# Kernel tuning notes

Measured on AMD Instinct MI355X. Metric: run time of the kernel, lower is better.

Reference implementation:

```python
import jax, jax.numpy as jnp
import numpy as np

N = 50000      # nodes
E = 800000     # edges
F = 64         # in_channels == out_channels
ED = 16        # edge_dim
G = 64         # graphs in batch
L = 2          # numLayers
BN_EPS = 1e-5
STD_EPS = 1e-5
AGG_DIM = F * 4 * 3  # 4 aggregators x 3 scalers


def setup_inputs() -> dict:
    key = jax.random.key(0)
    ks = jax.random.split(key, 12)
    r = lambda k, shp, fan: (jax.random.normal(k, shp, jnp.float32) / np.sqrt(fan)).astype(jnp.float32)
    return dict(
        x=jax.random.normal(ks[0], (N, F), jnp.float32),
        edge_attr=jax.random.normal(ks[1], (E, ED), jnp.float32),
        We=r(ks[2], (L, ED, F), ED), be=jnp.zeros((L, F), jnp.float32),
        Wpre=r(ks[3], (L, 3 * F, F), 3 * F), bpre=jnp.zeros((L, F), jnp.float32),
        Wpost=r(ks[4], (L, F + AGG_DIM, F), F + AGG_DIM), bpost=jnp.zeros((L, F), jnp.float32),
        Wlin=r(ks[5], (L, F, F), F), blin=jnp.zeros((L, F), jnp.float32),
        gamma=jnp.ones((L, F), jnp.float32), beta=jnp.zeros((L, F), jnp.float32),
        W1=r(ks[6], (F, 40), F), b1=jnp.zeros((40,), jnp.float32),
        W2=r(ks[7], (40, 1), 40), b2=jnp.zeros((1,), jnp.float32),
        edge_index=jax.random.randint(ks[8], (2, E), 0, N),
        batch=jnp.sort(jax.random.randint(ks[9], (N,), 0, G)),
    )


def _ceal_conv(x, src, dst, edge_attr, We, be, Wpre, bpre, Wpost, bpost, Wlin, blin, deg, amp, att):
    # PNA-style conv, towers=1, pre_layers=post_layers=1
    e = edge_attr @ We + be                                              # [E,F]
    h = jnp.concatenate([x[dst], x[src], e], axis=-1) @ Wpre + bpre      # [E,F]
    degc = jnp.maximum(deg, 1.0)[:, None]
    mean = jax.ops.segment_sum(h, dst, num_segments=N) / degc
    sq = jax.ops.segment_sum(h * h, dst, num_segments=N) / degc
    std = jnp.sqrt(jax.nn.relu(sq - mean * mean) + STD_EPS)
    has = (deg > 0)[:, None]
    mn = jnp.where(has, jax.ops.segment_min(h, dst, num_segments=N), 0.0)
    mx = jnp.where(has, jax.ops.segment_max(h, dst, num_segments=N), 0.0)
    aggs = jnp.concatenate([mean, mn, mx, std], axis=-1)                 # [N,4F]
    scaled = jnp.concatenate([aggs, aggs * amp[:, None], aggs * att[:, None]], axis=-1)  # [N,12F]
    out = jnp.concatenate([x, scaled], axis=-1) @ Wpost + bpost          # [N,F]
    return out @ Wlin + blin


def _bn(x, gamma, beta):
    mu = x.mean(0)
    var = x.var(0)  # biased, as torch BatchNorm training-mode normalization
    return (x - mu) * jax.lax.rsqrt(var + BN_EPS) * gamma + beta


def reference(x, edge_attr, We, be, Wpre, bpre, Wpost, bpost, Wlin, blin,
              gamma, beta, W1, b1, W2, b2, edge_index, batch):
    src, dst = edge_index[0], edge_index[1]
    deg = jax.ops.segment_sum(jnp.ones((E,), jnp.float32), dst, num_segments=N)
    avg_log = jnp.mean(jnp.log(deg + 1.0))
    logd = jnp.log(jnp.maximum(deg, 1.0) + 1.0)
    amp = logd / avg_log
    att = avg_log / logd
    for l in range(L):
        x = _ceal_conv(x, src, dst, edge_attr, We[l], be[l], Wpre[l], bpre[l],
                       Wpost[l], bpost[l], Wlin[l], blin[l], deg, amp, att)
        x = jax.nn.relu(_bn(x, gamma[l], beta[l]))
    cnt = jnp.maximum(jax.ops.segment_sum(jnp.ones((N,), jnp.float32), batch, num_segments=G), 1.0)
    gm = jax.ops.segment_sum(x, batch, num_segments=G) / cnt[:, None]    # global_mean_pool [G,F]
    return jax.nn.relu(gm @ W1 + b1) @ W2 + b2                           # [G,1]
```

## Files before the change

kernel.cpp:

```cpp
#include <hip/hip_runtime.h>
#include <math.h>
#include <float.h>

#define NN 50000
#define EE 800000
#define FF 64
#define EDIM 16
#define GG 64
#define NB64 782
#define NSB 196

typedef short bf16x8 __attribute__((ext_vector_type(8)));
typedef float f32x4 __attribute__((ext_vector_type(4)));

__device__ inline unsigned short bf_rne(float v) {
  unsigned int u = __float_as_uint(v);
  unsigned int r = (u + 0x7FFFu + ((u >> 16) & 1u)) >> 16;
  return (unsigned short)r;
}
__device__ inline float bf_up(unsigned short h) {
  return __uint_as_float(((unsigned int)h) << 16);
}
__device__ inline void split4(float4 v, ushort4& h, ushort4& l) {
  h.x = bf_rne(v.x); h.y = bf_rne(v.y); h.z = bf_rne(v.z); h.w = bf_rne(v.w);
  l.x = bf_rne(v.x - bf_up(h.x));
  l.y = bf_rne(v.y - bf_up(h.y));
  l.z = bf_rne(v.z - bf_up(h.z));
  l.w = bf_rne(v.w - bf_up(h.w));
}
__device__ inline float blo(unsigned int u) { return __uint_as_float(u << 16); }
__device__ inline float bhi(unsigned int u) { return __uint_as_float(u & 0xFFFF0000u); }

__global__ void k_deg(const int* __restrict__ eidx, int* __restrict__ deg) {
  int e = blockIdx.x * 256 + threadIdx.x;
  if (e < EE) atomicAdd(&deg[eidx[EE + e]], 1);
}

__global__ __launch_bounds__(256) void k_scanA(const int* __restrict__ deg, int* __restrict__ offsets,
                                               int* __restrict__ bsum, float* __restrict__ lsum) {
  __shared__ int ws[4];
  __shared__ float lw[4];
  int t = threadIdx.x;
  int lane = t & 63;
  int wv = t >> 6;
  int i = blockIdx.x * 256 + t;
  int v = (i < NN) ? deg[i] : 0;
  float lg = (i < NN) ? logf((float)v + 1.0f) : 0.0f;
  int x = v;
  #pragma unroll
  for (int o = 1; o < 64; o <<= 1) {
    int y = __shfl_up(x, o);
    if (lane >= o) x += y;
  }
  #pragma unroll
  for (int o = 1; o < 64; o <<= 1) lg += __shfl_xor(lg, o);
  if (lane == 63) ws[wv] = x;
  if (lane == 0) lw[wv] = lg;
  __syncthreads();
  int pre = 0;
  for (int k = 0; k < wv; k++) pre += ws[k];
  if (i < NN) offsets[i] = pre + x - v;
  if (t == 0) {
    bsum[blockIdx.x] = ws[0] + ws[1] + ws[2] + ws[3];
    lsum[blockIdx.x] = lw[0] + lw[1] + lw[2] + lw[3];
  }
}

__global__ __launch_bounds__(256) void k_scanB(const int* __restrict__ bsum, const float* __restrict__ lsum,
                                               int* __restrict__ bpref, float* __restrict__ meta,
                                               float* __restrict__ scbA) {
  __shared__ int ws[4];
  __shared__ float lw[4];
  int t = threadIdx.x;
  int lane = t & 63;
  int wv = t >> 6;
  int v = (t < NSB) ? bsum[t] : 0;
  float lg = (t < NSB) ? lsum[t] : 0.0f;
  int x = v;
  #pragma unroll
  for (int o = 1; o < 64; o <<= 1) {
    int y = __shfl_up(x, o);
    if (lane >= o) x += y;
  }
  #pragma unroll
  for (int o = 1; o < 64; o <<= 1) lg += __shfl_xor(lg, o);
  if (lane == 63) ws[wv] = x;
  if (lane == 0) lw[wv] = lg;
  __syncthreads();
  int pre = 0;
  for (int k = 0; k < wv; k++) pre += ws[k];
  if (t < NSB) bpref[t] = pre + x - v;
  if (t == 0) meta[0] = (lw[0] + lw[1] + lw[2] + lw[3]) / (float)NN;
  if (t < 64) { scbA[t] = 1.0f; scbA[64 + t] = 0.0f; }
  if (t == 0) scbA[128] = -FLT_MAX;
}

__global__ __launch_bounds__(256) void k_scanC(int* __restrict__ offsets, const int* __restrict__ bpref,
                                               const int* __restrict__ deg, const float* __restrict__ meta,
                                               float* __restrict__ amp, float* __restrict__ att) {
  int i = blockIdx.x * 256 + threadIdx.x;
  if (i < NN) {
    offsets[i] += bpref[blockIdx.x];
    float d = (float)deg[i];
    float avg = meta[0];
    float logd = logf(fmaxf(d, 1.0f) + 1.0f);
    amp[i] = logd / avg;
    att[i] = avg / logd;
  }
  if (i == 0) offsets[NN] = EE;
}

__global__ void k_scatter(const int* __restrict__ eidx, const int* __restrict__ offsets,
                          int* __restrict__ cursor, int* __restrict__ srcs,
                          const float* __restrict__ eattr, unsigned int* __restrict__ PermEA) {
  int e = blockIdx.x * 256 + threadIdx.x;
  if (e < EE) {
    int s = eidx[e];
    int d = eidx[EE + e];
    int pos = offsets[d] + atomicAdd(&cursor[d], 1);
    srcs[pos] = s;
    const float4* ep = (const float4*)(eattr + (size_t)e * EDIM);
    float4 q0 = ep[0], q1 = ep[1], q2 = ep[2], q3 = ep[3];
    uint4 pa, pb;
    pa.x = (unsigned)bf_rne(q0.x) | ((unsigned)bf_rne(q0.y) << 16);
    pa.y = (unsigned)bf_rne(q0.z) | ((unsigned)bf_rne(q0.w) << 16);
    pa.z = (unsigned)bf_rne(q1.x) | ((unsigned)bf_rne(q1.y) << 16);
    pa.w = (unsigned)bf_rne(q1.z) | ((unsigned)bf_rne(q1.w) << 16);
    pb.x = (unsigned)bf_rne(q2.x) | ((unsigned)bf_rne(q2.y) << 16);
    pb.y = (unsigned)bf_rne(q2.z) | ((unsigned)bf_rne(q2.w) << 16);
    pb.z = (unsigned)bf_rne(q3.x) | ((unsigned)bf_rne(q3.y) << 16);
    pb.w = (unsigned)bf_rne(q3.z) | ((unsigned)bf_rne(q3.w) << 16);
    ((uint4*)PermEA)[(size_t)pos * 2] = pa;
    ((uint4*)PermEA)[(size_t)pos * 2 + 1] = pb;
  }
}

__global__ __launch_bounds__(256) void k_prep2(const float* __restrict__ We, const float* __restrict__ be,
                                               const float* __restrict__ Wpre, const float* __restrict__ bpre,
                                               const float* __restrict__ Wpost, const float* __restrict__ bpost,
                                               const float* __restrict__ Wlin, const float* __restrict__ blin,
                                               unsigned short* __restrict__ MwT_h, unsigned short* __restrict__ MwT_l,
                                               float* __restrict__ bconst,
                                               unsigned short* __restrict__ WcT_h, unsigned short* __restrict__ WcT_l,
                                               unsigned short* __restrict__ WxT_h, unsigned short* __restrict__ WxT_l,
                                               float* __restrict__ bcomb) {
  int id = blockIdx.x * 256 + threadIdx.x;
  if (id < 53248) {
    int k = id >> 6, f = id & 63;
    float a = 0.0f;
    for (int j = 0; j < FF; j++) a += Wpost[(size_t)k * FF + j] * Wlin[j * FF + f];
    unsigned short h = bf_rne(a);
    WcT_h[f * 832 + k] = h;
    WcT_l[f * 832 + k] = bf_rne(a - bf_up(h));
  } else if (id < 61440) {
    int lid = id - 53248;
    int j = lid >> 6, k = lid & 63;
    float v = (j < 64) ? Wpre[k * FF + j] : Wpre[(64 + k) * FF + (j - 64)];
    unsigned short h = bf_rne(v);
    WxT_h[j * 64 + k] = h;
    WxT_l[j * 64 + k] = bf_rne(v - bf_up(h));
  } else if (id < 62464) {
    int lid = id - 61440;
    int k = lid >> 6, f = lid & 63;
    float a = 0.0f;
    for (int j = 0; j < FF; j++) a += We[k * FF + j] * Wpre[(128 + j) * FF + f];
    unsigned short h = bf_rne(a);
    int ct = f & 3, jcol = f >> 2;
    MwT_h[(ct * 16 + jcol) * 16 + k] = h;
    MwT_l[(ct * 16 + jcol) * 16 + k] = bf_rne(a - bf_up(h));
  } else {
    int f = threadIdx.x;
    if (blockIdx.x == 244 && f < 64) {
      float b = bpre[f];
      for (int j = 0; j < FF; j++) b += be[j] * Wpre[(128 + j) * FF + f];
      bconst[f] = b;
      float c = blin[f];
      for (int j = 0; j < FF; j++) c += bpost[j] * Wlin[j * FF + f];
      bcomb[f] = c;
    }
  }
}

__global__ __launch_bounds__(256) void k_xform(const float* __restrict__ x, const float* __restrict__ scb,
                                               const unsigned short* __restrict__ WxT_h,
                                               const unsigned short* __restrict__ WxT_l,
                                               float* __restrict__ Xd, unsigned short* __restrict__ Xs) {
  __shared__ unsigned short Ah[64 * 72], Al[64 * 72];
  __shared__ unsigned short Bh[128 * 72], Bl[128 * 72];
  int t = threadIdx.x;
  int n0 = blockIdx.x * 64;
  {
    int j = t >> 1, half = t & 1;
    const ushort4* srch = (const ushort4*)(WxT_h + j * 64 + half * 32);
    const ushort4* srcl = (const ushort4*)(WxT_l + j * 64 + half * 32);
    #pragma unroll
    for (int i = 0; i < 8; i++) {
      *(ushort4*)&Bh[j * 72 + half * 32 + i * 4] = srch[i];
      *(ushort4*)&Bl[j * 72 + half * 32 + i * 4] = srcl[i];
    }
  }
  {
    int r = t >> 2, c0 = (t & 3) * 16;
    int n = n0 + r;
    bool rok = n < NN;
    const float4* src = (const float4*)(x + (size_t)n * FF + c0);
    float flr = scb[128];
    #pragma unroll
    for (int c4 = 0; c4 < 4; c4++) {
      float4 v = rok ? src[c4] : make_float4(0.f, 0.f, 0.f, 0.f);
      float4 sc = ((const float4*)scb)[(c0 >> 2) + c4];
      float4 of = ((const float4*)(scb + 64))[(c0 >> 2) + c4];
      v.x = fmaxf(v.x * sc.x + of.x, flr);
      v.y = fmaxf(v.y * sc.y + of.y, flr);
      v.z = fmaxf(v.z * sc.z + of.z, flr);
      v.w = fmaxf(v.w * sc.w + of.w, flr);
      ushort4 h4, l4;
      split4(v, h4, l4);
      *(ushort4*)&Ah[r * 72 + c0 + c4 * 4] = h4;
      *(ushort4*)&Al[r * 72 + c0 + c4 * 4] = l4;
    }
  }
  __syncthreads();
  int lane = t & 63;
  int l15 = lane & 15;
  int quad = lane >> 4;
  int w = __builtin_amdgcn_readfirstlane(t >> 6);
  int rbase = (w & 1) * 32;
  int cbase = (w >> 1) * 64;
  f32x4 acc[2][4];
  #pragma unroll
  for (int rt = 0; rt < 2; rt++)
    #pragma unroll
    for (int ct = 0; ct < 4; ct++) acc[rt][ct] = (f32x4){0.f, 0.f, 0.f, 0.f};

  #pragma unroll
  for (int ks = 0; ks < 2; ks++) {
    bf16x8 a_h[2], a_l[2];
    #pragma unroll
    for (int rt = 0; rt < 2; rt++) {
      int row = rbase + rt * 16 + l15;
      a_h[rt] = *(const bf16x8*)&Ah[row * 72 + ks * 32 + quad * 8];
      a_l[rt] = *(const bf16x8*)&Al[row * 72 + ks * 32 + quad * 8];
    }
    #pragma unroll
    for (int ct = 0; ct < 4; ct++) {
      int col = cbase + ct * 16 + l15;
      bf16x8 b_h = *(const bf16x8*)&Bh[col * 72 + ks * 32 + quad * 8];
      bf16x8 b_l = *(const bf16x8*)&Bl[col * 72 + ks * 32 + quad * 8];
      #pragma unroll
      for (int rt = 0; rt < 2; rt++) {
        acc[rt][ct] = __builtin_amdgcn_mfma_f32_16x16x32_bf16(a_h[rt], b_h, acc[rt][ct], 0, 0, 0);
        acc[rt][ct] = __builtin_amdgcn_mfma_f32_16x16x32_bf16(a_h[rt], b_l, acc[rt][ct], 0, 0, 0);
        acc[rt][ct] = __builtin_amdgcn_mfma_f32_16x16x32_bf16(a_l[rt], b_h, acc[rt][ct], 0, 0, 0);
      }
    }
  }
  #pragma unroll
  for (int rt = 0; rt < 2; rt++) {
    #pragma unroll
    for (int ct = 0; ct < 4; ct++) {
      int col = cbase + ct * 16 + l15;
      #pragma unroll
      for (int reg = 0; reg < 4; reg++) {
        int n = n0 + rbase + rt * 16 + quad * 4 + reg;
        if (n < NN) {
          float v = acc[rt][ct][reg];
          if (col < 64) Xd[(size_t)n * FF + col] = v;
          else          Xs[(size_t)n * FF + (col - 64)] = bf_rne(v);
        }
      }
    }
  }
}

__global__ __launch_bounds__(256) void k_agg(const int* __restrict__ srcs, const int* __restrict__ offsets,
                                             const unsigned int* __restrict__ PermEA,
                                             const unsigned short* __restrict__ MwT_h,
                                             const unsigned short* __restrict__ MwT_l,
                                             const float* __restrict__ bconst,
                                             const float* __restrict__ Xd, const unsigned short* __restrict__ Xs,
                                             unsigned short* __restrict__ aggs) {
  int wid = __builtin_amdgcn_readfirstlane(threadIdx.x >> 6);
  int lane = threadIdx.x & 63;
  int l15 = lane & 15;
  int quad = lane >> 4;
  int n = blockIdx.x * 4 + wid;
  if (n >= NN) return;

  bf16x8 bh[4], bl[4];
  #pragma unroll
  for (int ct = 0; ct < 4; ct++) {
    if (quad < 2) {
      bh[ct] = *(const bf16x8*)&MwT_h[(ct * 16 + l15) * 16 + quad * 8];
      bl[ct] = *(const bf16x8*)&MwT_l[(ct * 16 + l15) * 16 + quad * 8];
    } else {
      bh[ct] = (bf16x8){0, 0, 0, 0, 0, 0, 0, 0};
      bl[ct] = (bf16x8){0, 0, 0, 0, 0, 0, 0, 0};
    }
  }

  float4 xd4 = *(const float4*)(Xd + (size_t)n * FF + 4 * l15);
  float4 bc4 = *(const float4*)(bconst + 4 * l15);
  float bas[4] = {xd4.x + bc4.x, xd4.y + bc4.y, xd4.z + bc4.z, xd4.w + bc4.w};

  int o0 = offsets[n], o1 = offsets[n + 1];
  float s[4]  = {0.f, 0.f, 0.f, 0.f};
  float sq[4] = {0.f, 0.f, 0.f, 0.f};
  float mn[4] = {FLT_MAX, FLT_MAX, FLT_MAX, FLT_MAX};
  float mx[4] = {-FLT_MAX, -FLT_MAX, -FLT_MAX, -FLT_MAX};

  for (int base = o0; base < o1; base += 16) {
    bf16x8 af = (bf16x8){0, 0, 0, 0, 0, 0, 0, 0};
    if (quad < 2) af = *(const bf16x8*)(PermEA + (size_t)(base + l15) * 8 + quad * 4);
    f32x4 acc[4];
    #pragma unroll
    for (int ct = 0; ct < 4; ct++) {
      f32x4 a = (f32x4){0.f, 0.f, 0.f, 0.f};
      a = __builtin_amdgcn_mfma_f32_16x16x32_bf16(af, bl[ct], a, 0, 0, 0);
      a = __builtin_amdgcn_mfma_f32_16x16x32_bf16(af, bh[ct], a, 0, 0, 0);
      acc[ct] = a;
    }
    #pragma unroll
    for (int reg = 0; reg < 4; reg++) {
      int e = base + quad * 4 + reg;
      bool valid = e < o1;
      int ec = min(e, o1 - 1);
      int src = srcs[ec];
      ushort4 xs4 = *(const ushort4*)(Xs + (size_t)src * FF + 4 * l15);
      float xf[4] = {bf_up(xs4.x), bf_up(xs4.y), bf_up(xs4.z), bf_up(xs4.w)};
      #pragma unroll
      for (int ct = 0; ct < 4; ct++) {
        float h = bas[ct] + xf[ct] + acc[ct][reg];
        float hv = valid ? h : 0.0f;
        s[ct] += hv;
        sq[ct] = fmaf(hv, hv, sq[ct]);
        float t1 = fminf(mn[ct], h);
        float t2 = fmaxf(mx[ct], h);
        mn[ct] = valid ? t1 : mn[ct];
        mx[ct] = valid ? t2 : mx[ct];
      }
    }
  }

  #pragma unroll
  for (int ct = 0; ct < 4; ct++) {
    s[ct] += __shfl_xor(s[ct], 16);  s[ct] += __shfl_xor(s[ct], 32);
    sq[ct] += __shfl_xor(sq[ct], 16); sq[ct] += __shfl_xor(sq[ct], 32);
    mn[ct] = fminf(mn[ct], __shfl_xor(mn[ct], 16)); mn[ct] = fminf(mn[ct], __shfl_xor(mn[ct], 32));
    mx[ct] = fmaxf(mx[ct], __shfl_xor(mx[ct], 16)); mx[ct] = fmaxf(mx[ct], __shfl_xor(mx[ct], 32));
  }

  float d = (float)(o1 - o0);
  float dc = fmaxf(d, 1.0f);
  float rdc = 1.0f / dc;
  bool has = d > 0.0f;
  ushort4 outv;
  unsigned short ov[4];
  #pragma unroll
  for (int ct = 0; ct < 4; ct++) {
    float mean = s[ct] * rdc;
    float msq = sq[ct] * rdc;
    float sd = sqrtf(fmaxf(msq - mean * mean, 0.0f) + 1e-5f);
    float vmn = has ? mn[ct] : 0.0f;
    float vmx = has ? mx[ct] : 0.0f;
    float val = (quad == 0) ? mean : (quad == 1) ? vmn : (quad == 2) ? vmx : sd;
    ov[ct] = bf_rne(val);
  }
  outv.x = ov[0]; outv.y = ov[1]; outv.z = ov[2]; outv.w = ov[3];
  *(ushort4*)(aggs + (size_t)n * 256 + quad * 64 + 4 * l15) = outv;
}

__global__ __launch_bounds__(256) void k_post(const float* __restrict__ x, const float* __restrict__ scb,
                                              const unsigned short* __restrict__ aggs,
                                              const float* __restrict__ amp, const float* __restrict__ att,
                                              const unsigned short* __restrict__ WcT_h,
                                              const unsigned short* __restrict__ WcT_l,
                                              const float* __restrict__ bcomb,
                                              float* __restrict__ y, float* __restrict__ partials) {
  __shared__ unsigned short Ah[64 * 72], Al[64 * 72];
  __shared__ unsigned short Bh[64 * 72], Bl[64 * 72];
  __shared__ float red_s[4][32], red_q[4][32];
  int t = threadIdx.x;
  int n0 = blockIdx.x * 64;
  int lane = t & 63;
  int l15 = lane & 15;
  int quad = lane >> 4;
  int w = __builtin_amdgcn_readfirstlane(t >> 6);
  int rbase = (w & 1) * 32;
  int cbase = (w >> 1) * 32;

  int ar = t >> 2;
  int ac0 = (t & 3) * 16;
  int an = n0 + ar;
  bool rok = an < NN;
  float sc_amp = rok ? amp[an] : 0.f;
  float sc_att = rok ? att[an] : 0.f;
  const float* xrow = x + (size_t)an * FF;
  const unsigned short* arow = aggs + (size_t)an * 256;
  float flr = scb[128];

  f32x4 acc[2][2];
  #pragma unroll
  for (int rt = 0; rt < 2; rt++)
    #pragma unroll
    for (int ct = 0; ct < 2; ct++) acc[rt][ct] = (f32x4){0.f, 0.f, 0.f, 0.f};

  for (int kc = 0; kc < 13; kc++) {
    if (kc == 0) {
      #pragma unroll
      for (int c4 = 0; c4 < 4; c4++) {
        float4 v = rok ? *(const float4*)(xrow + ac0 + c4 * 4) : make_float4(0.f, 0.f, 0.f, 0.f);
        float4 sc = ((const float4*)scb)[(ac0 >> 2) + c4];
        float4 of = ((const float4*)(scb + 64))[(ac0 >> 2) + c4];
        v.x = fmaxf(v.x * sc.x + of.x, flr);
        v.y = fmaxf(v.y * sc.y + of.y, flr);
        v.z = fmaxf(v.z * sc.z + of.z, flr);
        v.w = fmaxf(v.w * sc.w + of.w, flr);
        ushort4 h4, l4;
        split4(v, h4, l4);
        *(ushort4*)&Ah[ar * 72 + ac0 + c4 * 4] = h4;
        *(ushort4*)&Al[ar * 72 + ac0 + c4 * 4] = l4;
      }
    } else {
      int kcm = kc - 1;
      const unsigned short* srcb = arow + (kcm & 3) * 64;
      int sel = kcm >> 2;
      float scale = (sel == 0) ? 1.0f : (sel == 1 ? sc_amp : sc_att);
      #pragma unroll
      for (int c4 = 0; c4 < 4; c4++) {
        ushort4 u = rok ? *(const ushort4*)(srcb + ac0 + c4 * 4) : make_ushort4(0, 0, 0, 0);
        ushort4 h4;
        h4.x = bf_rne(bf_up(u.x) * scale);
        h4.y = bf_rne(bf_up(u.y) * scale);
        h4.z = bf_rne(bf_up(u.z) * scale);
        h4.w = bf_rne(bf_up(u.w) * scale);
        *(ushort4*)&Ah[ar * 72 + ac0 + c4 * 4] = h4;
      }
    }
    {
      int kbase = kc * 64;
      const ushort4* sh = (const ushort4*)(WcT_h + ar * 832 + kbase + ac0);
      const ushort4* sl = (const ushort4*)(WcT_l + ar * 832 + kbase + ac0);
      #pragma unroll
      for (int i = 0; i < 4; i++) {
        *(ushort4*)&Bh[ar * 72 + ac0 + i * 4] = sh[i];
        *(ushort4*)&Bl[ar * 72 + ac0 + i * 4] = sl[i];
      }
    }
    __syncthreads();
    bool full = (kc == 0);
    #pragma unroll
    for (int ks = 0; ks < 2; ks++) {
      bf16x8 a_h[2], a_l[2], b_h[2], b_l[2];
      #pragma unroll
      for (int rt = 0; rt < 2; rt++) {
        int row = rbase + rt * 16 + l15;
        a_h[rt] = *(const bf16x8*)&Ah[row * 72 + ks * 32 + quad * 8];
        if (full) a_l[rt] = *(const bf16x8*)&Al[row * 72 + ks * 32 + quad * 8];
      }
      #pragma unroll
      for (int ct = 0; ct < 2; ct++) {
        int col = cbase + ct * 16 + l15;
        b_h[ct] = *(const bf16x8*)&Bh[col * 72 + ks * 32 + quad * 8];
        b_l[ct] = *(const bf16x8*)&Bl[col * 72 + ks * 32 + quad * 8];
      }
      #pragma unroll
      for (int rt = 0; rt < 2; rt++)
        #pragma unroll
        for (int ct = 0; ct < 2; ct++) {
          acc[rt][ct] = __builtin_amdgcn_mfma_f32_16x16x32_bf16(a_h[rt], b_h[ct], acc[rt][ct], 0, 0, 0);
          acc[rt][ct] = __builtin_amdgcn_mfma_f32_16x16x32_bf16(a_h[rt], b_l[ct], acc[rt][ct], 0, 0, 0);
          if (full)
            acc[rt][ct] = __builtin_amdgcn_mfma_f32_16x16x32_bf16(a_l[rt], b_h[ct], acc[rt][ct], 0, 0, 0);
        }
    }
    __syncthreads();
  }

  float ps[2] = {0.f, 0.f}, pq[2] = {0.f, 0.f};
  #pragma unroll
  for (int ct = 0; ct < 2; ct++) {
    int col = cbase + ct * 16 + l15;
    float bc = bcomb[col];
    #pragma unroll
    for (int rt = 0; rt < 2; rt++) {
      #pragma unroll
      for (int reg = 0; reg < 4; reg++) {
        int n = n0 + rbase + rt * 16 + quad * 4 + reg;
        float v = acc[rt][ct][reg] + bc;
        if (n < NN) {
          y[(size_t)n * FF + col] = v;
          ps[ct] += v;
          pq[ct] += v * v;
        }
      }
    }
  }
  #pragma unroll
  for (int ct = 0; ct < 2; ct++) {
    ps[ct] += __shfl_xor(ps[ct], 16);
    ps[ct] += __shfl_xor(ps[ct], 32);
    pq[ct] += __shfl_xor(pq[ct], 16);
    pq[ct] += __shfl_xor(pq[ct], 32);
  }
  if (quad == 0) {
    #pragma unroll
    for (int ct = 0; ct < 2; ct++) {
      red_s[w][ct * 16 + l15] = ps[ct];
      red_q[w][ct * 16 + l15] = pq[ct];
    }
  }
  __syncthreads();
  if (t < 64) {
    float ss, qq;
    if (t < 32) { ss = red_s[0][t] + red_s[1][t]; qq = red_q[0][t] + red_q[1][t]; }
    else        { ss = red_s[2][t - 32] + red_s[3][t - 32]; qq = red_q[2][t - 32] + red_q[3][t - 32]; }
    partials[(size_t)blockIdx.x * 128 + t] = ss;
    partials[(size_t)blockIdx.x * 128 + 64 + t] = qq;
  }
}

__global__ __launch_bounds__(1024) void k_bnfin(const float* __restrict__ partials,
                                                const float* __restrict__ gamma, const float* __restrict__ beta,
                                                float* __restrict__ scb) {
  __shared__ float red[1024];
  __shared__ double tot[128];
  int t = threadIdx.x;
  int c = t & 127, seg = t >> 7;
  float s = 0.f;
  for (int i = seg; i < NB64; i += 8) s += partials[(size_t)i * 128 + c];
  red[t] = s;
  __syncthreads();
  if (t < 128) {
    double d = 0.0;
    #pragma unroll
    for (int sg = 0; sg < 8; sg++) d += (double)red[sg * 128 + t];
    tot[t] = d;
  }
  __syncthreads();
  if (t < 64) {
    double mu = tot[t] / (double)NN;
    double var = tot[64 + t] / (double)NN - mu * mu;
    float sc = gamma[t] * rsqrtf((float)fmax(var, 0.0) + 1e-5f);
    scb[t] = sc;
    scb[64 + t] = beta[t] - (float)mu * sc;
  }
  if (t == 0) scb[128] = 0.0f;
}

__global__ __launch_bounds__(256) void k_pool(const float* __restrict__ x, const float* __restrict__ scb,
                                              const int* __restrict__ batch,
                                              float* __restrict__ psum, float* __restrict__ cnt) {
  int lane = threadIdx.x & 63;
  int wv = threadIdx.x >> 6;
  int wglobal = blockIdx.x * 4 + wv;
  int nw = gridDim.x * 4;
  int per = (NN + nw - 1) / nw;
  int n0 = wglobal * per;
  int n1 = min(n0 + per, NN);
  if (n0 >= n1) return;
  float sc = scb[lane], of = scb[64 + lane], flr = scb[128];
  int gcur = batch[n0];
  float acc = 0.0f;
  int count = 0;
  for (int n = n0; n < n1; n++) {
    int g = batch[n];
    float v = fmaxf(x[(size_t)n * FF + lane] * sc + of, flr);
    if (g != gcur) {
      atomicAdd(&psum[gcur * FF + lane], acc);
      if (lane == 0) atomicAdd(&cnt[gcur], (float)count);
      gcur = g; acc = 0.0f; count = 0;
    }
    acc += v;
    count++;
  }
  atomicAdd(&psum[gcur * FF + lane], acc);
  if (lane == 0) atomicAdd(&cnt[gcur], (float)count);
}

__global__ void k_final(const float* __restrict__ psum, const float* __restrict__ cnt,
                        const float* __restrict__ W1, const float* __restrict__ b1,
                        const float* __restrict__ W2, const float* __restrict__ b2, float* __restrict__ out) {
  int g = threadIdx.x;
  if (g >= GG) return;
  float c = fmaxf(cnt[g], 1.0f);
  float gm[64];
  #pragma unroll
  for (int i = 0; i < 64; i++) gm[i] = psum[g * FF + i] / c;
  float o = b2[0];
  for (int h = 0; h < 40; h++) {
    float a = b1[h];
    #pragma unroll
    for (int i = 0; i < 64; i++) a += gm[i] * W1[i * 40 + h];
    o += fmaxf(a, 0.0f) * W2[h];
  }
  out[g] = o;
}

extern "C" void kernel_launch(void* const* d_in, const int* in_sizes, int n_in,
                              void* d_out, int out_size, void* d_ws, size_t ws_size,
                              hipStream_t stream) {
  (void)in_sizes; (void)n_in; (void)out_size; (void)ws_size;
  const float* x0    = (const float*)d_in[0];
  const float* eattr = (const float*)d_in[1];
  const float* We    = (const float*)d_in[2];
  const float* be    = (const float*)d_in[3];
  const float* Wpre  = (const float*)d_in[4];
  const float* bpre  = (const float*)d_in[5];
  const float* Wpost = (const float*)d_in[6];
  const float* bpost = (const float*)d_in[7];
  const float* Wlin  = (const float*)d_in[8];
  const float* blin  = (const float*)d_in[9];
  const float* gamma = (const float*)d_in[10];
  const float* beta  = (const float*)d_in[11];
  const float* W1    = (const float*)d_in[12];
  const float* b1    = (const float*)d_in[13];
  const float* W2    = (const float*)d_in[14];
  const float* b2    = (const float*)d_in[15];
  const int* eidx    = (const int*)d_in[16];
  const int* batch   = (const int*)d_in[17];
  float* out = (float*)d_out;

  char* w = (char*)d_ws;
  size_t off = 0;
  auto alloc = [&](size_t bytes) -> void* {
    void* p = w + off;
    off += bytes;
    off = (off + 255) & ~(size_t)255;
    return p;
  };
  int*    deg     = (int*)alloc(NN * sizeof(int));
  int*    offsets = (int*)alloc((NN + 1) * sizeof(int));
  int*    cursor  = (int*)alloc(NN * sizeof(int));
  int*    srcs    = (int*)alloc(EE * sizeof(int));
  unsigned int* PermEA = (unsigned int*)alloc(((size_t)EE + 16) * 8 * sizeof(unsigned int));
  int*    bsum    = (int*)alloc(NSB * sizeof(int));
  int*    bpref   = (int*)alloc(NSB * sizeof(int));
  float*  lsum    = (float*)alloc(NSB * sizeof(float));
  float*  meta    = (float*)alloc(sizeof(float));
  float*  amp     = (float*)alloc(NN * sizeof(float));
  float*  att     = (float*)alloc(NN * sizeof(float));
  unsigned short* MwT_h = (unsigned short*)alloc(FF * EDIM * sizeof(unsigned short));
  unsigned short* MwT_l = (unsigned short*)alloc(FF * EDIM * sizeof(unsigned short));
  float*  bconst  = (float*)alloc(FF * sizeof(float));
  float*  bcomb   = (float*)alloc(FF * sizeof(float));
  float*  scbA    = (float*)alloc(129 * sizeof(float));
  float*  scbB    = (float*)alloc(2 * 129 * sizeof(float));
  unsigned short* WcT_h = (unsigned short*)alloc(FF * 832 * sizeof(unsigned short));
  unsigned short* WcT_l = (unsigned short*)alloc(FF * 832 * sizeof(unsigned short));
  unsigned short* WxT_h = (unsigned short*)alloc(128 * 64 * sizeof(unsigned short));
  unsigned short* WxT_l = (unsigned short*)alloc(128 * 64 * sizeof(unsigned short));
  float*  partials = (float*)alloc((size_t)NB64 * 128 * sizeof(float));
  float*  Xd      = (float*)alloc((size_t)NN * FF * sizeof(float));
  unsigned short* Xs = (unsigned short*)alloc((size_t)NN * FF * sizeof(unsigned short));
  unsigned short* aggs = (unsigned short*)alloc((size_t)NN * 256 * sizeof(unsigned short));
  float*  ybuf    = (float*)alloc((size_t)NN * FF * sizeof(float));
  float*  psum    = (float*)alloc((GG * FF + GG) * sizeof(float));
  float*  cnt     = psum + GG * FF;

  hipMemsetAsync(deg, 0, NN * sizeof(int), stream);
  hipMemsetAsync(cursor, 0, NN * sizeof(int), stream);
  hipMemsetAsync(psum, 0, (GG * FF + GG) * sizeof(float), stream);

  k_deg<<<(EE + 255) / 256, 256, 0, stream>>>(eidx, deg);
  k_scanA<<<NSB, 256, 0, stream>>>(deg, offsets, bsum, lsum);
  k_scanB<<<1, 256, 0, stream>>>(bsum, lsum, bpref, meta, scbA);
  k_scanC<<<NSB, 256, 0, stream>>>(offsets, bpref, deg, meta, amp, att);
  k_scatter<<<(EE + 255) / 256, 256, 0, stream>>>(eidx, offsets, cursor, srcs, eattr, PermEA);

  const float* xin = x0;
  const float* scb_in = scbA;
  for (int l = 0; l < 2; l++) {
    k_prep2<<<245, 256, 0, stream>>>(We + l * EDIM * FF, be + l * FF, Wpre + (size_t)l * 3 * FF * FF,
                                     bpre + l * FF, Wpost + (size_t)l * 832 * FF, bpost + l * FF,
                                     Wlin + l * FF * FF, blin + l * FF,
                                     MwT_h, MwT_l, bconst, WcT_h, WcT_l, WxT_h, WxT_l, bcomb);
    k_xform<<<NB64, 256, 0, stream>>>(xin, scb_in, WxT_h, WxT_l, Xd, Xs);
    k_agg<<<(NN + 3) / 4, 256, 0, stream>>>(srcs, offsets, PermEA, MwT_h, MwT_l, bconst, Xd, Xs, aggs);
    k_post<<<NB64, 256, 0, stream>>>(xin, scb_in, aggs, amp, att, WcT_h, WcT_l, bcomb, ybuf, partials);
    k_bnfin<<<1, 1024, 0, stream>>>(partials, gamma + l * FF, beta + l * FF, scbB + l * 129);
    xin = ybuf;
    scb_in = scbB + l * 129;
  }
  k_pool<<<200, 256, 0, stream>>>(ybuf, scbB + 129, batch, psum, cnt);
  k_final<<<1, 64, 0, stream>>>(psum, cnt, W1, b1, W2, b2, out);
}
```

Baseline: 552.3 us.

## Process two destination nodes per wavefront in aggregation kernel with vectorized src loads

Each wavefront in the aggregation kernel now handles two consecutive destination nodes, interleaving their edge chunks in one loop so that loads for both nodes can be in flight together. Source indices are read as one int4 per quad instead of four clamped scalar loads, and the srcs buffer is padded and zeroed to keep those vector reads in bounds. The per-node bias is folded into the MFMA accumulator's initial value, removing an add per element. The goal is more memory-level parallelism and less per-node fixed overhead. The cost is more register pressure, half as many blocks, and imbalance when the two nodes have different degrees.

Measured after the change: 554.5 us. No clear change (+0.4%).

```diff
diff --git a/kernel.cpp b/kernel.cpp
--- a/kernel.cpp
+++ b/kernel.cpp
@@ -284,8 +284,10 @@
   int lane = threadIdx.x & 63;
   int l15 = lane & 15;
   int quad = lane >> 4;
-  int n = blockIdx.x * 4 + wid;
-  if (n >= NN) return;
+  int nA = blockIdx.x * 8 + wid * 2;
+  if (nA >= NN) return;
+  int nB = nA + 1;
+  bool hasB = nB < NN;
 
   bf16x8 bh[4], bl[4];
   #pragma unroll
@@ -299,75 +301,155 @@
     }
   }
 
-  float4 xd4 = *(const float4*)(Xd + (size_t)n * FF + 4 * l15);
+  int o0A = offsets[nA];
+  int o1A = offsets[nA + 1];
+  int o0B = o1A;
+  int o1B = hasB ? offsets[nB + 1] : o1A;
+
   float4 bc4 = *(const float4*)(bconst + 4 * l15);
-  float bas[4] = {xd4.x + bc4.x, xd4.y + bc4.y, xd4.z + bc4.z, xd4.w + bc4.w};
-
-  int o0 = offsets[n], o1 = offsets[n + 1];
-  float s[4]  = {0.f, 0.f, 0.f, 0.f};
-  float sq[4] = {0.f, 0.f, 0.f, 0.f};
-  float mn[4] = {FLT_MAX, FLT_MAX, FLT_MAX, FLT_MAX};
-  float mx[4] = {-FLT_MAX, -FLT_MAX, -FLT_MAX, -FLT_MAX};
-
-  for (int base = o0; base < o1; base += 16) {
-    bf16x8 af = (bf16x8){0, 0, 0, 0, 0, 0, 0, 0};
-    if (quad < 2) af = *(const bf16x8*)(PermEA + (size_t)(base + l15) * 8 + quad * 4);
-    f32x4 acc[4];
+  float4 xdA = *(const float4*)(Xd + (size_t)nA * FF + 4 * l15);
+  float4 xdB = hasB ? *(const float4*)(Xd + (size_t)nB * FF + 4 * l15) : make_float4(0.f, 0.f, 0.f, 0.f);
+  float basA[4] = {xdA.x + bc4.x, xdA.y + bc4.y, xdA.z + bc4.z, xdA.w + bc4.w};
+  float basB[4] = {xdB.x + bc4.x, xdB.y + bc4.y, xdB.z + bc4.z, xdB.w + bc4.w};
+
+  float sA[4] = {0.f, 0.f, 0.f, 0.f}, sqA[4] = {0.f, 0.f, 0.f, 0.f};
+  float mnA[4] = {FLT_MAX, FLT_MAX, FLT_MAX, FLT_MAX}, mxA[4] = {-FLT_MAX, -FLT_MAX, -FLT_MAX, -FLT_MAX};
+  float sB[4] = {0.f, 0.f, 0.f, 0.f}, sqB[4] = {0.f, 0.f, 0.f, 0.f};
+  float mnB[4] = {FLT_MAX, FLT_MAX, FLT_MAX, FLT_MAX}, mxB[4] = {-FLT_MAX, -FLT_MAX, -FLT_MAX, -FLT_MAX};
+
+  for (int t = 0;; t++) {
+    int baseA = o0A + t * 16;
+    int baseB = o0B + t * 16;
+    bool doA = baseA < o1A;
+    bool doB = hasB && (baseB < o1B);
+    if (!(doA | doB)) break;
+
+    bf16x8 afA = (bf16x8){0, 0, 0, 0, 0, 0, 0, 0};
+    bf16x8 afB = (bf16x8){0, 0, 0, 0, 0, 0, 0, 0};
+    int4 svA = make_int4(0, 0, 0, 0), svB = make_int4(0, 0, 0, 0);
+    if (doA) {
+      if (quad < 2) afA = *(const bf16x8*)(PermEA + (size_t)(baseA + l15) * 8 + quad * 4);
+      svA = *(const int4*)(srcs + baseA + quad * 4);
+    }
+    if (doB) {
+      if (quad < 2) afB = *(const bf16x8*)(PermEA + (size_t)(baseB + l15) * 8 + quad * 4);
+      svB = *(const int4*)(srcs + baseB + quad * 4);
+    }
+
+    if (doA) {
+      f32x4 acc[4];
+      #pragma unroll
+      for (int ct = 0; ct < 4; ct++) {
+        f32x4 a = (f32x4){basA[ct], basA[ct], basA[ct], basA[ct]};
+        a = __builtin_amdgcn_mfma_f32_16x16x32_bf16(afA, bl[ct], a, 0, 0, 0);
+        a = __builtin_amdgcn_mfma_f32_16x16x32_bf16(afA, bh[ct], a, 0, 0, 0);
+        acc[ct] = a;
+      }
+      const int* svp = &svA.x;
+      #pragma unroll
+      for (int reg = 0; reg < 4; reg++) {
+        int e = baseA + quad * 4 + reg;
+        bool valid = e < o1A;
+        int src = svp[reg];
+        ushort4 xs4 = *(const ushort4*)(Xs + (size_t)src * FF + 4 * l15);
+        float xf[4] = {bf_up(xs4.x), bf_up(xs4.y), bf_up(xs4.z), bf_up(xs4.w)};
+        #pragma unroll
+        for (int ct = 0; ct < 4; ct++) {
+          float h = xf[ct] + acc[ct][reg];
+          float hv = valid ? h : 0.0f;
+          sA[ct] += hv;
+          sqA[ct] = fmaf(hv, hv, sqA[ct]);
+          float t1 = fminf(mnA[ct], h);
+          float t2 = fmaxf(mxA[ct], h);
+          mnA[ct] = valid ? t1 : mnA[ct];
+          mxA[ct] = valid ? t2 : mxA[ct];
+        }
+      }
+    }
+    if (doB) {
+      f32x4 acc[4];
+      #pragma unroll
+      for (int ct = 0; ct < 4; ct++) {
+        f32x4 a = (f32x4){basB[ct], basB[ct], basB[ct], basB[ct]};
+        a = __builtin_amdgcn_mfma_f32_16x16x32_bf16(afB, bl[ct], a, 0, 0, 0);
+        a = __builtin_amdgcn_mfma_f32_16x16x32_bf16(afB, bh[ct], a, 0, 0, 0);
+        acc[ct] = a;
+      }
+      const int* svp = &svB.x;
+      #pragma unroll
+      for (int reg = 0; reg < 4; reg++) {
+        int e = baseB + quad * 4 + reg;
+        bool valid = e < o1B;
+        int src = svp[reg];
+        ushort4 xs4 = *(const ushort4*)(Xs + (size_t)src * FF + 4 * l15);
+        float xf[4] = {bf_up(xs4.x), bf_up(xs4.y), bf_up(xs4.z), bf_up(xs4.w)};
+        #pragma unroll
+        for (int ct = 0; ct < 4; ct++) {
+          float h = xf[ct] + acc[ct][reg];
+          float hv = valid ? h : 0.0f;
+          sB[ct] += hv;
+          sqB[ct] = fmaf(hv, hv, sqB[ct]);
+          float t1 = fminf(mnB[ct], h);
+          float t2 = fmaxf(mxB[ct], h);
+          mnB[ct] = valid ? t1 : mnB[ct];
+          mxB[ct] = valid ? t2 : mxB[ct];
+        }
+      }
+    }
+  }
+
+  #pragma unroll
+  for (int ct = 0; ct < 4; ct++) {
+    sA[ct] += __shfl_xor(sA[ct], 16);  sA[ct] += __shfl_xor(sA[ct], 32);
+    sqA[ct] += __shfl_xor(sqA[ct], 16); sqA[ct] += __shfl_xor(sqA[ct], 32);
+    mnA[ct] = fminf(mnA[ct], __shfl_xor(mnA[ct], 16)); mnA[ct] = fminf(mnA[ct], __shfl_xor(mnA[ct], 32));
+    mxA[ct] = fmaxf(mxA[ct], __shfl_xor(mxA[ct], 16)); mxA[ct] = fmaxf(mxA[ct], __shfl_xor(mxA[ct], 32));
+  }
+  {
+    float d = (float)(o1A - o0A);
+    float dc = fmaxf(d, 1.0f);
+    float rdc = 1.0f / dc;
+    bool has = d > 0.0f;
+    unsigned short ov[4];
     #pragma unroll
     for (int ct = 0; ct < 4; ct++) {
-      f32x4 a = (f32x4){0.f, 0.f, 0.f, 0.f};
-      a = __builtin_amdgcn_mfma_f32_16x16x32_bf16(af, bl[ct], a, 0, 0, 0);
-      a = __builtin_amdgcn_mfma_f32_16x16x32_bf16(af, bh[ct], a, 0, 0, 0);
-      acc[ct] = a;
-    }
-    #pragma unroll
-    for (int reg = 0; reg < 4; reg++) {
-      int e = base + quad * 4 + reg;
-      bool valid = e < o1;
-      int ec = min(e, o1 - 1);
-      int src = srcs[ec];
-      ushort4 xs4 = *(const ushort4*)(Xs + (size_t)src * FF + 4 * l15);
-      float xf[4] = {bf_up(xs4.x), bf_up(xs4.y), bf_up(xs4.z), bf_up(xs4.w)};
-      #pragma unroll
-      for (int ct = 0; ct < 4; ct++) {
-        float h = bas[ct] + xf[ct] + acc[ct][reg];
-        float hv = valid ? h : 0.0f;
-        s[ct] += hv;
-        sq[ct] = fmaf(hv, hv, sq[ct]);
-        float t1 = fminf(mn[ct], h);
-        float t2 = fmaxf(mx[ct], h);
-        mn[ct] = valid ? t1 : mn[ct];
-        mx[ct] = valid ? t2 : mx[ct];
-      }
-    }
-  }
-
-  #pragma unroll
-  for (int ct = 0; ct < 4; ct++) {
-    s[ct] += __shfl_xor(s[ct], 16);  s[ct] += __shfl_xor(s[ct], 32);
-    sq[ct] += __shfl_xor(sq[ct], 16); sq[ct] += __shfl_xor(sq[ct], 32);
-    mn[ct] = fminf(mn[ct], __shfl_xor(mn[ct], 16)); mn[ct] = fminf(mn[ct], __shfl_xor(mn[ct], 32));
-    mx[ct] = fmaxf(mx[ct], __shfl_xor(mx[ct], 16)); mx[ct] = fmaxf(mx[ct], __shfl_xor(mx[ct], 32));
-  }
-
-  float d = (float)(o1 - o0);
-  float dc = fmaxf(d, 1.0f);
-  float rdc = 1.0f / dc;
-  bool has = d > 0.0f;
-  ushort4 outv;
-  unsigned short ov[4];
-  #pragma unroll
-  for (int ct = 0; ct < 4; ct++) {
-    float mean = s[ct] * rdc;
-    float msq = sq[ct] * rdc;
-    float sd = sqrtf(fmaxf(msq - mean * mean, 0.0f) + 1e-5f);
-    float vmn = has ? mn[ct] : 0.0f;
-    float vmx = has ? mx[ct] : 0.0f;
-    float val = (quad == 0) ? mean : (quad == 1) ? vmn : (quad == 2) ? vmx : sd;
-    ov[ct] = bf_rne(val);
-  }
-  outv.x = ov[0]; outv.y = ov[1]; outv.z = ov[2]; outv.w = ov[3];
-  *(ushort4*)(aggs + (size_t)n * 256 + quad * 64 + 4 * l15) = outv;
+      float mean = sA[ct] * rdc;
+      float msq = sqA[ct] * rdc;
+      float sd = sqrtf(fmaxf(msq - mean * mean, 0.0f) + 1e-5f);
+      float vmn = has ? mnA[ct] : 0.0f;
+      float vmx = has ? mxA[ct] : 0.0f;
+      float val = (quad == 0) ? mean : (quad == 1) ? vmn : (quad == 2) ? vmx : sd;
+      ov[ct] = bf_rne(val);
+    }
+    ushort4 outv; outv.x = ov[0]; outv.y = ov[1]; outv.z = ov[2]; outv.w = ov[3];
+    *(ushort4*)(aggs + (size_t)nA * 256 + quad * 64 + 4 * l15) = outv;
+  }
+  if (hasB) {
+    #pragma unroll
+    for (int ct = 0; ct < 4; ct++) {
+      sB[ct] += __shfl_xor(sB[ct], 16);  sB[ct] += __shfl_xor(sB[ct], 32);
+      sqB[ct] += __shfl_xor(sqB[ct], 16); sqB[ct] += __shfl_xor(sqB[ct], 32);
+      mnB[ct] = fminf(mnB[ct], __shfl_xor(mnB[ct], 16)); mnB[ct] = fminf(mnB[ct], __shfl_xor(mnB[ct], 32));
+      mxB[ct] = fmaxf(mxB[ct], __shfl_xor(mxB[ct], 16)); mxB[ct] = fmaxf(mxB[ct], __shfl_xor(mxB[ct], 32));
+    }
+    float d = (float)(o1B - o0B);
+    float dc = fmaxf(d, 1.0f);
+    float rdc = 1.0f / dc;
+    bool has = d > 0.0f;
+    unsigned short ov[4];
+    #pragma unroll
+    for (int ct = 0; ct < 4; ct++) {
+      float mean = sB[ct] * rdc;
+      float msq = sqB[ct] * rdc;
+      float sd = sqrtf(fmaxf(msq - mean * mean, 0.0f) + 1e-5f);
+      float vmn = has ? mnB[ct] : 0.0f;
+      float vmx = has ? mxB[ct] : 0.0f;
+      float val = (quad == 0) ? mean : (quad == 1) ? vmn : (quad == 2) ? vmx : sd;
+      ov[ct] = bf_rne(val);
+    }
+    ushort4 outv; outv.x = ov[0]; outv.y = ov[1]; outv.z = ov[2]; outv.w = ov[3];
+    *(ushort4*)(aggs + (size_t)nB * 256 + quad * 64 + 4 * l15) = outv;
+  }
 }
 
 __global__ __launch_bounds__(256) void k_post(const float* __restrict__ x, const float* __restrict__ scb,
@@ -632,7 +714,7 @@
   int*    deg     = (int*)alloc(NN * sizeof(int));
   int*    offsets = (int*)alloc((NN + 1) * sizeof(int));
   int*    cursor  = (int*)alloc(NN * sizeof(int));
-  int*    srcs    = (int*)alloc(EE * sizeof(int));
+  int*    srcs    = (int*)alloc((EE + 16) * sizeof(int));
   unsigned int* PermEA = (unsigned int*)alloc(((size_t)EE + 16) * 8 * sizeof(unsigned int));
   int*    bsum    = (int*)alloc(NSB * sizeof(int));
   int*    bpref   = (int*)alloc(NSB * sizeof(int));
@@ -660,6 +742,7 @@
 
   hipMemsetAsync(deg, 0, NN * sizeof(int), stream);
   hipMemsetAsync(cursor, 0, NN * sizeof(int), stream);
+  hipMemsetAsync(srcs + EE, 0, 16 * sizeof(int), stream);
   hipMemsetAsync(psum, 0, (GG * FF + GG) * sizeof(float), stream);
 
   k_deg<<<(EE + 255) / 256, 256, 0, stream>>>(eidx, deg);
@@ -676,7 +759,7 @@
                                      Wlin + l * FF * FF, blin + l * FF,
                                      MwT_h, MwT_l, bconst, WcT_h, WcT_l, WxT_h, WxT_l, bcomb);
     k_xform<<<NB64, 256, 0, stream>>>(xin, scb_in, WxT_h, WxT_l, Xd, Xs);
-    k_agg<<<(NN + 3) / 4, 256, 0, stream>>>(srcs, offsets, PermEA, MwT_h, MwT_l, bconst, Xd, Xs, aggs);
+    k_agg<<<(NN + 7) / 8, 256, 0, stream>>>(srcs, offsets, PermEA, MwT_h, MwT_l, bconst, Xd, Xs, aggs);
     k_post<<<NB64, 256, 0, stream>>>(xin, scb_in, aggs, amp, att, WcT_h, WcT_l, bcomb, ybuf, partials);
     k_bnfin<<<1, 1024, 0, stream>>>(partials, gamma + l * FF, beta + l * FF, scbB + l * 129);
     xin = ybuf;
```

## Factor amp/att scalers out of post GEMM and read weights directly from global

Applied to the files above, without the earlier changes.

k_post no longer builds scaled copies of the aggregates per k-chunk. It keeps three accumulator sets (plain, amp-scaled, att-scaled), loads the aggregate A fragments directly from global memory, and applies amp and att per row in the epilogue. Both k_xform and k_post now read the B weight fragments straight from global or L2 instead of staging them in shared memory, which removes the per-chunk __syncthreads. This trades LDS traffic and barriers for more register pressure and uncoalesced but cache-resident global loads. It also pads srcs with 16 zeroed entries.

Measured after the change: 608.5 us. 1.1x slower.

```diff
diff --git a/kernel.cpp b/kernel.cpp
--- a/kernel.cpp
+++ b/kernel.cpp
@@ -186,19 +186,8 @@
                                                const unsigned short* __restrict__ WxT_l,
                                                float* __restrict__ Xd, unsigned short* __restrict__ Xs) {
   __shared__ unsigned short Ah[64 * 72], Al[64 * 72];
-  __shared__ unsigned short Bh[128 * 72], Bl[128 * 72];
   int t = threadIdx.x;
   int n0 = blockIdx.x * 64;
-  {
-    int j = t >> 1, half = t & 1;
-    const ushort4* srch = (const ushort4*)(WxT_h + j * 64 + half * 32);
-    const ushort4* srcl = (const ushort4*)(WxT_l + j * 64 + half * 32);
-    #pragma unroll
-    for (int i = 0; i < 8; i++) {
-      *(ushort4*)&Bh[j * 72 + half * 32 + i * 4] = srch[i];
-      *(ushort4*)&Bl[j * 72 + half * 32 + i * 4] = srcl[i];
-    }
-  }
   {
     int r = t >> 2, c0 = (t & 3) * 16;
     int n = n0 + r;
@@ -245,8 +234,8 @@
     #pragma unroll
     for (int ct = 0; ct < 4; ct++) {
       int col = cbase + ct * 16 + l15;
-      bf16x8 b_h = *(const bf16x8*)&Bh[col * 72 + ks * 32 + quad * 8];
-      bf16x8 b_l = *(const bf16x8*)&Bl[col * 72 + ks * 32 + quad * 8];
+      bf16x8 b_h = *(const bf16x8*)(WxT_h + (size_t)col * 64 + ks * 32 + quad * 8);
+      bf16x8 b_l = *(const bf16x8*)(WxT_l + (size_t)col * 64 + ks * 32 + quad * 8);
       #pragma unroll
       for (int rt = 0; rt < 2; rt++) {
         acc[rt][ct] = __builtin_amdgcn_mfma_f32_16x16x32_bf16(a_h[rt], b_h, acc[rt][ct], 0, 0, 0);
@@ -378,7 +367,6 @@
                                               const float* __restrict__ bcomb,
                                               float* __restrict__ y, float* __restrict__ partials) {
   __shared__ unsigned short Ah[64 * 72], Al[64 * 72];
-  __shared__ unsigned short Bh[64 * 72], Bl[64 * 72];
   __shared__ float red_s[4][32], red_q[4][32];
   int t = threadIdx.x;
   int n0 = blockIdx.x * 64;
@@ -389,107 +377,108 @@
   int rbase = (w & 1) * 32;
   int cbase = (w >> 1) * 32;
 
-  int ar = t >> 2;
-  int ac0 = (t & 3) * 16;
-  int an = n0 + ar;
-  bool rok = an < NN;
-  float sc_amp = rok ? amp[an] : 0.f;
-  float sc_att = rok ? att[an] : 0.f;
-  const float* xrow = x + (size_t)an * FF;
-  const unsigned short* arow = aggs + (size_t)an * 256;
-  float flr = scb[128];
-
-  f32x4 acc[2][2];
-  #pragma unroll
-  for (int rt = 0; rt < 2; rt++)
-    #pragma unroll
-    for (int ct = 0; ct < 2; ct++) acc[rt][ct] = (f32x4){0.f, 0.f, 0.f, 0.f};
-
-  for (int kc = 0; kc < 13; kc++) {
-    if (kc == 0) {
-      #pragma unroll
-      for (int c4 = 0; c4 < 4; c4++) {
-        float4 v = rok ? *(const float4*)(xrow + ac0 + c4 * 4) : make_float4(0.f, 0.f, 0.f, 0.f);
-        float4 sc = ((const float4*)scb)[(ac0 >> 2) + c4];
-        float4 of = ((const float4*)(scb + 64))[(ac0 >> 2) + c4];
-        v.x = fmaxf(v.x * sc.x + of.x, flr);
-        v.y = fmaxf(v.y * sc.y + of.y, flr);
-        v.z = fmaxf(v.z * sc.z + of.z, flr);
-        v.w = fmaxf(v.w * sc.w + of.w, flr);
-        ushort4 h4, l4;
-        split4(v, h4, l4);
-        *(ushort4*)&Ah[ar * 72 + ac0 + c4 * 4] = h4;
-        *(ushort4*)&Al[ar * 72 + ac0 + c4 * 4] = l4;
+  {
+    int ar = t >> 2;
+    int ac0 = (t & 3) * 16;
+    int an = n0 + ar;
+    bool rok = an < NN;
+    const float* xrow = x + (size_t)an * FF;
+    float flr = scb[128];
+    #pragma unroll
+    for (int c4 = 0; c4 < 4; c4++) {
+      float4 v = rok ? *(const float4*)(xrow + ac0 + c4 * 4) : make_float4(0.f, 0.f, 0.f, 0.f);
+      float4 sc = ((const float4*)scb)[(ac0 >> 2) + c4];
+      float4 of = ((const float4*)(scb + 64))[(ac0 >> 2) + c4];
+      v.x = fmaxf(v.x * sc.x + of.x, flr);
+      v.y = fmaxf(v.y * sc.y + of.y, flr);
+      v.z = fmaxf(v.z * sc.z + of.z, flr);
+      v.w = fmaxf(v.w * sc.w + of.w, flr);
+      ushort4 h4, l4;
+      split4(v, h4, l4);
+      *(ushort4*)&Ah[ar * 72 + ac0 + c4 * 4] = h4;
+      *(ushort4*)&Al[ar * 72 + ac0 + c4 * 4] = l4;
+    }
+  }
+  __syncthreads();
+
+  f32x4 acc[3][2][2];
+  #pragma unroll
+  for (int s = 0; s < 3; s++)
+    #pragma unroll
+    for (int rt = 0; rt < 2; rt++)
+      #pragma unroll
+      for (int ct = 0; ct < 2; ct++) acc[s][rt][ct] = (f32x4){0.f, 0.f, 0.f, 0.f};
+
+  #pragma unroll
+  for (int ks = 0; ks < 2; ks++) {
+    bf16x8 a_h[2], a_l[2];
+    #pragma unroll
+    for (int rt = 0; rt < 2; rt++) {
+      int row = rbase + rt * 16 + l15;
+      a_h[rt] = *(const bf16x8*)&Ah[row * 72 + ks * 32 + quad * 8];
+      a_l[rt] = *(const bf16x8*)&Al[row * 72 + ks * 32 + quad * 8];
+    }
+    #pragma unroll
+    for (int ct = 0; ct < 2; ct++) {
+      int col = cbase + ct * 16 + l15;
+      bf16x8 b_h = *(const bf16x8*)(WcT_h + (size_t)col * 832 + ks * 32 + quad * 8);
+      bf16x8 b_l = *(const bf16x8*)(WcT_l + (size_t)col * 832 + ks * 32 + quad * 8);
+      #pragma unroll
+      for (int rt = 0; rt < 2; rt++) {
+        acc[0][rt][ct] = __builtin_amdgcn_mfma_f32_16x16x32_bf16(a_h[rt], b_h, acc[0][rt][ct], 0, 0, 0);
+        acc[0][rt][ct] = __builtin_amdgcn_mfma_f32_16x16x32_bf16(a_h[rt], b_l, acc[0][rt][ct], 0, 0, 0);
+        acc[0][rt][ct] = __builtin_amdgcn_mfma_f32_16x16x32_bf16(a_l[rt], b_h, acc[0][rt][ct], 0, 0, 0);
       }
-    } else {
-      int kcm = kc - 1;
-      const unsigned short* srcb = arow + (kcm & 3) * 64;
-      int sel = kcm >> 2;
-      float scale = (sel == 0) ? 1.0f : (sel == 1 ? sc_amp : sc_att);
-      #pragma unroll
-      for (int c4 = 0; c4 < 4; c4++) {
-        ushort4 u = rok ? *(const ushort4*)(srcb + ac0 + c4 * 4) : make_ushort4(0, 0, 0, 0);
-        ushort4 h4;
-        h4.x = bf_rne(bf_up(u.x) * scale);
-        h4.y = bf_rne(bf_up(u.y) * scale);
-        h4.z = bf_rne(bf_up(u.z) * scale);
-        h4.w = bf_rne(bf_up(u.w) * scale);
-        *(ushort4*)&Ah[ar * 72 + ac0 + c4 * 4] = h4;
+    }
+  }
+
+  #pragma unroll
+  for (int c = 0; c < 4; c++) {
+    #pragma unroll
+    for (int ks = 0; ks < 2; ks++) {
+      bf16x8 a[2];
+      #pragma unroll
+      for (int rt = 0; rt < 2; rt++) {
+        int row = n0 + rbase + rt * 16 + l15;
+        row = min(row, NN - 1);
+        a[rt] = *(const bf16x8*)(aggs + (size_t)row * 256 + c * 64 + ks * 32 + quad * 8);
       }
-    }
-    {
-      int kbase = kc * 64;
-      const ushort4* sh = (const ushort4*)(WcT_h + ar * 832 + kbase + ac0);
-      const ushort4* sl = (const ushort4*)(WcT_l + ar * 832 + kbase + ac0);
-      #pragma unroll
-      for (int i = 0; i < 4; i++) {
-        *(ushort4*)&Bh[ar * 72 + ac0 + i * 4] = sh[i];
-        *(ushort4*)&Bl[ar * 72 + ac0 + i * 4] = sl[i];
-      }
-    }
-    __syncthreads();
-    bool full = (kc == 0);
-    #pragma unroll
-    for (int ks = 0; ks < 2; ks++) {
-      bf16x8 a_h[2], a_l[2], b_h[2], b_l[2];
-      #pragma unroll
-      for (int rt = 0; rt < 2; rt++) {
-        int row = rbase + rt * 16 + l15;
-        a_h[rt] = *(const bf16x8*)&Ah[row * 72 + ks * 32 + quad * 8];
-        if (full) a_l[rt] = *(const bf16x8*)&Al[row * 72 + ks * 32 + quad * 8];
-      }
-      #pragma unroll
-      for (int ct = 0; ct < 2; ct++) {
-        int col = cbase + ct * 16 + l15;
-        b_h[ct] = *(const bf16x8*)&Bh[col * 72 + ks * 32 + quad * 8];
-        b_l[ct] = *(const bf16x8*)&Bl[col * 72 + ks * 32 + quad * 8];
-      }
-      #pragma unroll
-      for (int rt = 0; rt < 2; rt++)
+      #pragma unroll
+      for (int s = 0; s < 3; s++) {
+        int kb = 64 + s * 256 + c * 64 + ks * 32 + quad * 8;
         #pragma unroll
         for (int ct = 0; ct < 2; ct++) {
-          acc[rt][ct] = __builtin_amdgcn_mfma_f32_16x16x32_bf16(a_h[rt], b_h[ct], acc[rt][ct], 0, 0, 0);
-          acc[rt][ct] = __builtin_amdgcn_mfma_f32_16x16x32_bf16(a_h[rt], b_l[ct], acc[rt][ct], 0, 0, 0);
-          if (full)
-            acc[rt][ct] = __builtin_amdgcn_mfma_f32_16x16x32_bf16(a_l[rt], b_h[ct], acc[rt][ct], 0, 0, 0);
+          int col = cbase + ct * 16 + l15;
+          bf16x8 b_h = *(const bf16x8*)(WcT_h + (size_t)col * 832 + kb);
+          bf16x8 b_l = *(const bf16x8*)(WcT_l + (size_t)col * 832 + kb);
+          #pragma unroll
+          for (int rt = 0; rt < 2; rt++) {
+            acc[s][rt][ct] = __builtin_amdgcn_mfma_f32_16x16x32_bf16(a[rt], b_h, acc[s][rt][ct], 0, 0, 0);
+            acc[s][rt][ct] = __builtin_amdgcn_mfma_f32_16x16x32_bf16(a[rt], b_l, acc[s][rt][ct], 0, 0, 0);
+          }
         }
-    }
-    __syncthreads();
+      }
+    }
   }
 
   float ps[2] = {0.f, 0.f}, pq[2] = {0.f, 0.f};
-  #pragma unroll
-  for (int ct = 0; ct < 2; ct++) {
-    int col = cbase + ct * 16 + l15;
-    float bc = bcomb[col];
-    #pragma unroll
-    for (int rt = 0; rt < 2; rt++) {
-      #pragma unroll
-      for (int reg = 0; reg < 4; reg++) {
-        int n = n0 + rbase + rt * 16 + quad * 4 + reg;
-        float v = acc[rt][ct][reg] + bc;
-        if (n < NN) {
-          y[(size_t)n * FF + col] = v;
+  float bc[2];
+  #pragma unroll
+  for (int ct = 0; ct < 2; ct++) bc[ct] = bcomb[cbase + ct * 16 + l15];
+  #pragma unroll
+  for (int rt = 0; rt < 2; rt++) {
+    #pragma unroll
+    for (int reg = 0; reg < 4; reg++) {
+      int n = n0 + rbase + rt * 16 + quad * 4 + reg;
+      bool ok = n < NN;
+      int nc = min(n, NN - 1);
+      float am = amp[nc];
+      float at = att[nc];
+      #pragma unroll
+      for (int ct = 0; ct < 2; ct++) {
+        float v = acc[0][rt][ct][reg] + am * acc[1][rt][ct][reg] + at * acc[2][rt][ct][reg] + bc[ct];
+        if (ok) {
+          y[(size_t)n * FF + (cbase + ct * 16 + l15)] = v;
           ps[ct] += v;
           pq[ct] += v * v;
         }
@@ -632,7 +621,7 @@
   int*    deg     = (int*)alloc(NN * sizeof(int));
   int*    offsets = (int*)alloc((NN + 1) * sizeof(int));
   int*    cursor  = (int*)alloc(NN * sizeof(int));
-  int*    srcs    = (int*)alloc(EE * sizeof(int));
+  int*    srcs    = (int*)alloc((EE + 16) * sizeof(int));
   unsigned int* PermEA = (unsigned int*)alloc(((size_t)EE + 16) * 8 * sizeof(unsigned int));
   int*    bsum    = (int*)alloc(NSB * sizeof(int));
   int*    bpref   = (int*)alloc(NSB * sizeof(int));
@@ -660,6 +649,7 @@
 
   hipMemsetAsync(deg, 0, NN * sizeof(int), stream);
   hipMemsetAsync(cursor, 0, NN * sizeof(int), stream);
+  hipMemsetAsync(srcs + EE, 0, 16 * sizeof(int), stream);
   hipMemsetAsync(psum, 0, (GG * FF + GG) * sizeof(float), stream);
 
   k_deg<<<(EE + 255) / 256, 256, 0, stream>>>(eidx, deg);
```
